# Optimization experiments

Hardware: AMD Instinct MI355X
Metric: run time of the kernel (lower is better)

Reference implementation:

```python
import jax, jax.numpy as jnp
import numpy as np
import math

BS, S, E, H, DK = 32, 512, 512, 8, 64


def setup_inputs() -> dict:
    key = jax.random.key(0)
    ks = jax.random.split(key, 10)
    q = jax.random.normal(ks[0], (BS, S, E), jnp.float32)
    k = jax.random.normal(ks[1], (BS, S, E), jnp.float32)
    v = jax.random.normal(ks[2], (BS, S, E), jnp.float32)
    # strictly-causal mask: allowed where col < row (np.triu(k=0)==0)
    mask = jnp.tril(jnp.ones((S, S), bool), -1)[None, None]
    sc = 1.0 / math.sqrt(E)  # xavier-ish scale for square linears
    Wq = jax.random.normal(ks[3], (E, E), jnp.float32) * sc
    Wk = jax.random.normal(ks[4], (E, E), jnp.float32) * sc
    Wv = jax.random.normal(ks[5], (E, E), jnp.float32) * sc
    Wo = jax.random.normal(ks[6], (E, E), jnp.float32) * sc
    bq = jnp.zeros((E,), jnp.float32)
    bk = jnp.zeros((E,), jnp.float32)
    bv = jnp.zeros((E,), jnp.float32)
    bo = jnp.zeros((E,), jnp.float32)
    gammas = jax.random.normal(ks[7], (H, 1, 1), jnp.float32) * 0.5
    return {"q": q, "k": k, "v": v, "mask": mask, "zero_pad": 1,
            "Wq": Wq, "bq": bq, "Wk": Wk, "bk": bk, "Wv": Wv, "bv": bv,
            "Wo": Wo, "bo": bo, "gammas": gammas}


def reference(q, k, v, mask, zero_pad, Wq, bq, Wk, bk, Wv, bv, Wo, bo, gammas):
    bs = q.shape[0]
    # projections (torch Linear: x @ W.T + b), split heads -> [b,h,s,d]
    def heads(x, W, b):
        return (x @ W.T + b).reshape(bs, S, H, DK).transpose(0, 2, 1, 3)
    qh, kh, vh = heads(q, Wq, bq), heads(k, Wk, bk), heads(v, Wv, bv)

    scores = jnp.einsum('bhqd,bhkd->bhqk', qh, kh) / math.sqrt(DK)

    # --- distance-decay term (no-grad in original) ---
    neg = jnp.float32(-1e32)
    scores_ = jnp.where(mask, scores, neg)
    scores_ = jax.nn.softmax(scores_, axis=-1) * mask.astype(scores.dtype)
    distcum = jnp.cumsum(scores_, axis=-1)
    disttotal = jnp.sum(scores_, axis=-1, keepdims=True)
    idx = jnp.arange(S)
    position_effect = jnp.abs(idx[None, :] - idx[:, None]).astype(scores.dtype)[None, None]
    dist_scores = jnp.sqrt(jnp.clip((disttotal - distcum) * position_effect, 0.0))
    dist_scores = jax.lax.stop_gradient(dist_scores)

    gamma = -jax.nn.softplus(gammas)[None]  # [1,h,1,1]
    total_effect = jnp.clip(jnp.exp(dist_scores * gamma), 1e-5, 1e5)

    scores = scores * total_effect
    scores = jnp.where(mask, scores, neg)
    scores = jax.nn.softmax(scores, axis=-1)
    if zero_pad:
        scores = scores.at[:, :, 0, :].set(0.0)

    out = jnp.einsum('bhqk,bhkd->bhqd', scores, vh)
    concat = out.transpose(0, 2, 1, 3).reshape(bs, S, E)
    return concat @ Wo.T + bo
```

## Files before the change

kernel.cpp:

```cpp
#include <hip/hip_runtime.h>
#include <hip/hip_bf16.h>
#include <hip/hip_fp16.h>
#include <stdint.h>

#define BSZ 32
#define SEQ 512
#define EMB 512
#define NH  8
#define DKD 64
#define LOG2E 1.4426950408889634f

typedef float f32x4 __attribute__((ext_vector_type(4)));
typedef short s16x8 __attribute__((ext_vector_type(8)));

#if __has_builtin(__builtin_amdgcn_exp2f)
#define EXP2(x) __builtin_amdgcn_exp2f(x)
#else
#define EXP2(x) exp2f(x)
#endif
#define RCP(x) __builtin_amdgcn_rcpf(x)

__device__ inline unsigned short f2bf(float f) {
  union { float f; unsigned u; } v; v.f = f;
  unsigned r = v.u + 0x7fffu + ((v.u >> 16) & 1u);
  return (unsigned short)(r >> 16);
}

__device__ inline ushort4 pack4bf(float4 v) {
  union { __hip_bfloat162 h2[2]; ushort4 u4; } cv;
  cv.h2[0] = __float22bfloat162_rn(make_float2(v.x, v.y));
  cv.h2[1] = __float22bfloat162_rn(make_float2(v.z, v.w));
  return cv.u4;
}

__device__ inline void stage16(const void* g, void* l) {
#if defined(__has_builtin) && __has_builtin(__builtin_amdgcn_global_load_lds)
  __builtin_amdgcn_global_load_lds(
      (const __attribute__((address_space(1))) void*)g,
      (__attribute__((address_space(3))) void*)l, 16, 0, 0);
#else
  *reinterpret_cast<uint4*>(l) = *reinterpret_cast<const uint4*>(g);
#endif
}

template<int CTRL>
__device__ inline float dpp_shr_f(float x) {
  return __builtin_bit_cast(float,
    __builtin_amdgcn_update_dpp(0, __builtin_bit_cast(int, x), CTRL, 0xf, 0xf, true));
}
__device__ inline float rlane(float v, int l) {
  return __builtin_bit_cast(float, __builtin_amdgcn_readlane(__builtin_bit_cast(int, v), l));
}

__global__ __launch_bounds__(256)
void wcvt(const float* __restrict__ w0, const float* __restrict__ w1,
          const float* __restrict__ w2, const float* __restrict__ w3,
          unsigned short* __restrict__ o0, unsigned short* __restrict__ o1,
          unsigned short* __restrict__ o2, unsigned short* __restrict__ o3)
{
  const float* src = (blockIdx.y == 0) ? w0 : (blockIdx.y == 1) ? w1
                   : (blockIdx.y == 2) ? w2 : w3;
  unsigned short* dst = (blockIdx.y == 0) ? o0 : (blockIdx.y == 1) ? o1
                      : (blockIdx.y == 2) ? o2 : o3;
  const int i = (blockIdx.x * 256 + threadIdx.x) * 8;
  float4 a = *reinterpret_cast<const float4*>(src + i);
  float4 b = *reinterpret_cast<const float4*>(src + i + 4);
  union { ushort4 p[2]; s16x8 v; } cc;
  cc.p[0] = pack4bf(a); cc.p[1] = pack4bf(b);
  *reinterpret_cast<s16x8*>(dst + i) = cc.v;
}

template<int PROJ>
__global__ __launch_bounds__(256)
void proj_gemm(const float* __restrict__ A, const unsigned short* __restrict__ Bw,
               const float* __restrict__ bias, unsigned short* __restrict__ Out,
               float oscale)
{
  __shared__ __align__(16) char smem[32768];
  char* const sA = smem;
  char* const sB = smem + 16384;
  const int tid  = threadIdx.x;
  const int lane = tid & 63;
  const int w    = tid >> 6;
  const int lin  = blockIdx.x;
  const int x    = lin & 7;
  const int j    = lin >> 3;
  const int pl   = j & 15;
  const int m0   = (x * 16 + pl) * 128;
  const int n0   = (j >> 4) * 128;
  const int K = EMB;

  const int wr   = (w >> 1) * 64;
  const int wc   = (w & 1) * 64;
  const int base = w * 1024 + lane * 16;

  auto stage = [&](int k0) {
    #pragma unroll
    for (int c = 0; c < 4; ++c) {
      const int flat = c * 4096 + base;
      const int row  = flat >> 7;
      const int gl   = ((flat >> 4) & 7) ^ (row & 7);
      stage16(&A[(size_t)(m0 + row) * K + k0 + gl * 4], sA + flat);
    }
    #pragma unroll
    for (int c = 0; c < 2; ++c) {
      const int flat = c * 4096 + base;
      const int r    = flat >> 7;
      const int gl   = ((flat >> 4) & 7) ^ (r & 7);
      const int nn   = r + ((gl >> 2) << 6);
      stage16(&Bw[(size_t)(n0 + nn) * K + k0 + (gl & 3) * 8], sB + flat);
    }
  };

  f32x4 acc[4][4] = {};
  auto compute = [&]() {
    s16x8 af[4], bf[4];
    #pragma unroll
    for (int i = 0; i < 4; ++i) {
      const int row = wr + i * 16 + (lane & 15);
      const int g1  = (lane >> 4) << 1;
      float4 v1 = *reinterpret_cast<const float4*>(sA + row * 128 + ((g1 ^ (row & 7)) << 4));
      float4 v2 = *reinterpret_cast<const float4*>(sA + row * 128 + (((g1 + 1) ^ (row & 7)) << 4));
      union { ushort4 p[2]; s16x8 vv; } cc;
      cc.p[0] = pack4bf(v1); cc.p[1] = pack4bf(v2);
      af[i] = cc.vv;
    }
    #pragma unroll
    for (int jj = 0; jj < 4; ++jj) {
      const int n  = wc + jj * 16 + (lane & 15);
      const int r  = n & 63;
      const int gl = ((n >> 6) << 2) + (lane >> 4);
      bf[jj] = *reinterpret_cast<const s16x8*>(sB + r * 128 + ((gl ^ (r & 7)) << 4));
    }
    #pragma unroll
    for (int i = 0; i < 4; ++i)
      #pragma unroll
      for (int jj = 0; jj < 4; ++jj)
        acc[i][jj] = __builtin_amdgcn_mfma_f32_16x16x32_bf16(af[i], bf[jj], acc[i][jj], 0, 0, 0);
  };

  for (int t = 0; t < 16; ++t) {
    stage(t * 32);
    __syncthreads();
    compute();
    __syncthreads();
  }

  unsigned short* tl = (unsigned short*)smem;
  #pragma unroll
  for (int jj = 0; jj < 4; ++jj) {
    const int n  = wc + jj * 16 + (lane & 15);
    const float bs = bias[n0 + n];
    #pragma unroll
    for (int i = 0; i < 4; ++i)
      #pragma unroll
      for (int r = 0; r < 4; ++r) {
        const int m = wr + i * 16 + (lane >> 4) * 4 + r;
        const unsigned short val = f2bf((acc[i][jj][r] + bs) * oscale);
        const int row = (PROJ == 2) ? n : m;
        const int cb  = (PROJ == 2) ? (m * 2) : (n * 2);
        *(unsigned short*)((char*)tl + row * 256 + (cb ^ ((row & 7) << 4))) = val;
      }
  }
  __syncthreads();
  #pragma unroll
  for (int c = 0; c < 8; ++c) {
    const int flat = c * 4096 + tid * 16;
    const int rowi = flat >> 8;
    const int cb   = flat & 255;
    s16x8 vchunk = *reinterpret_cast<const s16x8*>(
        (char*)tl + rowi * 256 + (cb ^ ((rowi & 7) << 4)));
    size_t dst;
    if (PROJ == 2) {
      const int gn = n0 + rowi;
      const int b  = m0 >> 9, sb = (m0 & 511) + (cb >> 1);
      const int h  = gn >> 6, d = gn & 63;
      dst = ((size_t)(b * NH + h) * DKD + d) * SEQ + sb;
    } else {
      const int gm = m0 + rowi;
      const int gn = n0 + (cb >> 1);
      const int b  = gm >> 9, s = gm & 511;
      const int h  = gn >> 6, d = gn & 63;
      dst = ((size_t)(b * NH + h) * SEQ + s) * DKD + d;
    }
    *reinterpret_cast<s16x8*>(&Out[dst]) = vchunk;
  }
}

__global__ __launch_bounds__(256)
void out_gemm(const unsigned short* __restrict__ At,
              const unsigned short* __restrict__ Wo,
              const float* __restrict__ bo, float* __restrict__ C)
{
  __shared__ __align__(16) char smem[2 * 16384];
  const int tid  = threadIdx.x;
  const int lane = tid & 63;
  const int w    = tid >> 6;
  const int lin  = blockIdx.x;
  const int x    = lin & 7;
  const int j    = lin >> 3;
  const int P    = x * 16 + (j >> 2);
  const int m0   = P * 128;
  const int n0   = (j & 3) * 128;
  const int K = EMB, N = EMB;

  const int wr   = (w >> 1) * 64;
  const int wc   = (w & 1) * 64;
  const int base = w * 1024 + lane * 16;

  auto stage = [&](int buf, int k0) {
    char* sA = smem + buf * 16384;
    char* sB = sA + 8192;
    #pragma unroll
    for (int c = 0; c < 2; ++c) {
      const int flat = c * 4096 + base;
      const int r    = flat >> 7;
      const int gl   = ((flat >> 4) & 7) ^ (r & 7);
      const int row  = r + ((gl >> 2) << 6);
      stage16(&At[(size_t)(m0 + row) * K + k0 + (gl & 3) * 8], sA + flat);
    }
    #pragma unroll
    for (int c = 0; c < 2; ++c) {
      const int flat = c * 4096 + base;
      const int r    = flat >> 7;
      const int gl   = ((flat >> 4) & 7) ^ (r & 7);
      const int nn   = r + ((gl >> 2) << 6);
      stage16(&Wo[(size_t)(n0 + nn) * K + k0 + (gl & 3) * 8], sB + flat);
    }
  };

  f32x4 acc[4][4] = {};
  auto compute = [&](int buf) {
    char* sA = smem + buf * 16384;
    char* sB = sA + 8192;
    s16x8 af[4], bf[4];
    #pragma unroll
    for (int i = 0; i < 4; ++i) {
      const int row = wr + i * 16 + (lane & 15);
      const int r   = row & 63;
      const int gl  = ((row >> 6) << 2) + (lane >> 4);
      af[i] = *reinterpret_cast<const s16x8*>(sA + r * 128 + ((gl ^ (r & 7)) << 4));
    }
    #pragma unroll
    for (int jj = 0; jj < 4; ++jj) {
      const int n  = wc + jj * 16 + (lane & 15);
      const int r  = n & 63;
      const int gl = ((n >> 6) << 2) + (lane >> 4);
      bf[jj] = *reinterpret_cast<const s16x8*>(sB + r * 128 + ((gl ^ (r & 7)) << 4));
    }
    #pragma unroll
    for (int i = 0; i < 4; ++i)
      #pragma unroll
      for (int jj = 0; jj < 4; ++jj)
        acc[i][jj] = __builtin_amdgcn_mfma_f32_16x16x32_bf16(af[i], bf[jj], acc[i][jj], 0, 0, 0);
  };

  stage(0, 0);
  int cur = 0;
  for (int t = 0; t < 15; ++t) {
    stage(cur ^ 1, (t + 1) * 32);
    asm volatile("s_waitcnt vmcnt(4)" ::: "memory");
    __builtin_amdgcn_s_barrier();
    __builtin_amdgcn_sched_barrier(0);
    compute(cur);
    asm volatile("s_waitcnt lgkmcnt(0)" ::: "memory");
    __builtin_amdgcn_s_barrier();
    cur ^= 1;
  }
  asm volatile("s_waitcnt vmcnt(0)" ::: "memory");
  __builtin_amdgcn_s_barrier();
  __builtin_amdgcn_sched_barrier(0);
  compute(cur);

  #pragma unroll
  for (int i = 0; i < 4; ++i)
    #pragma unroll
    for (int jj = 0; jj < 4; ++jj)
      #pragma unroll
      for (int r = 0; r < 4; ++r) {
        const int gm = m0 + wr + i * 16 + (lane >> 4) * 4 + r;
        const int gn = n0 + wc + jj * 16 + (lane & 15);
        C[(size_t)gm * N + gn] = acc[i][jj][r] + bo[gn];
      }
}

template<int R>
__device__ inline void phase2_rows(unsigned short* s_lds, int w, int lane,
                                   int q0, int zp, float g2)
{
  constexpr int L  = 64 / R;
  constexpr int IT = 4 / R;
  const int seg = lane / L;
  const int li  = lane & (L - 1);
  const int jb  = li * 8;
  const float NEGINF = -__builtin_inff();
  #pragma unroll
  for (int it = 0; it < IT; ++it) {
    const int r  = w * 4 + it * R + seg;
    const int qg = q0 + r;
    const int gs = li ^ (r & 7);
    unsigned short* rowp = &s_lds[r * 512 + gs * 8];
    float pn2[8];
    if (qg == 0) {
      const float u = zp ? 0.0f : (1.0f / 512.0f);
      #pragma unroll
      for (int i = 0; i < 8; ++i) pn2[i] = u;
    } else {
      float sL[8];
      {
        s16x8 raw = *reinterpret_cast<const s16x8*>(rowp);
        union { s16x8 v; __half2 h[4]; } u; u.v = raw;
        #pragma unroll
        for (int i = 0; i < 4; ++i) {
          float2 f = __half22float2(u.h[i]);
          sL[2 * i] = f.x; sL[2 * i + 1] = f.y;
        }
      }
      #pragma unroll
      for (int i = 0; i < 8; ++i) sL[i] = (jb + i < qg) ? sL[i] : NEGINF;
      float p[8], c[8];
      float run = 0.f;
      #pragma unroll
      for (int i = 0; i < 8; ++i) { p[i] = EXP2(sL[i]); run += p[i]; c[i] = run; }
      float t = run;
      t += dpp_shr_f<0x111>(t);
      t += dpp_shr_f<0x112>(t);
      t += dpp_shr_f<0x114>(t);
      t += dpp_shr_f<0x118>(t);
      float tot;
      if constexpr (R == 1) {
        const float r0 = rlane(t, 15), r1 = rlane(t, 31), r2 = rlane(t, 47);
        const float a1 = r0, a2 = r0 + r1, a3 = a2 + r2;
        tot = a3 + rlane(t, 63);
        t += (lane >= 48) ? a3 : (lane >= 32) ? a2 : (lane >= 16) ? a1 : 0.f;
      } else if constexpr (R == 2) {
        const float r0 = rlane(t, 15), r2 = rlane(t, 47);
        t += (lane & 16) ? ((lane < 32) ? r0 : r2) : 0.f;
        tot = __shfl(t, lane | 31, 64);
      } else {
        tot = __shfl(t, lane | 15, 64);
      }
      const float pre  = tot - (t - run);
      const float g2r  = g2 * __builtin_amdgcn_sqrtf(RCP(tot));
      const float fb   = (float)(qg - jb);
      float p2[8]; float run2 = 0.f;
      #pragma unroll
      for (int i = 0; i < 8; ++i) {
        const float rem = pre - c[i];
        const float arg = fmaxf(rem * (fb - (float)i), 0.f);
        float te = EXP2(__builtin_amdgcn_sqrtf(arg) * g2r);
        te = fmaxf(te, 1e-5f);
        p2[i] = EXP2(sL[i] * te);
        run2 += p2[i];
      }
      float y = run2;
      y += dpp_shr_f<0x111>(y);
      y += dpp_shr_f<0x112>(y);
      y += dpp_shr_f<0x114>(y);
      y += dpp_shr_f<0x118>(y);
      float s2;
      if constexpr (R == 1) {
        s2 = rlane(y, 15) + rlane(y, 31) + rlane(y, 47) + rlane(y, 63);
      } else if constexpr (R == 2) {
        y += (lane & 16) ? ((lane < 32) ? rlane(y, 15) : rlane(y, 47)) : 0.f;
        s2 = __shfl(y, lane | 31, 64);
      } else {
        s2 = __shfl(y, lane | 15, 64);
      }
      const float inv2 = RCP(s2);
      #pragma unroll
      for (int i = 0; i < 8; ++i) pn2[i] = p2[i] * inv2;
    }
    union { __hip_bfloat162 h2[4]; uint4 u; } pk;
    pk.h2[0] = __float22bfloat162_rn(make_float2(pn2[0], pn2[1]));
    pk.h2[1] = __float22bfloat162_rn(make_float2(pn2[2], pn2[3]));
    pk.h2[2] = __float22bfloat162_rn(make_float2(pn2[4], pn2[5]));
    pk.h2[3] = __float22bfloat162_rn(make_float2(pn2[6], pn2[7]));
    *reinterpret_cast<uint4*>(rowp) = pk.u;
  }
}

__global__ __launch_bounds__(256)
void attn_kernel(const unsigned short* __restrict__ Qh,
                 const unsigned short* __restrict__ Kh,
                 const unsigned short* __restrict__ Vt,
                 unsigned short* __restrict__ Aout,
                 const float* __restrict__ gammas,
                 const int* __restrict__ zero_pad)
{
  __shared__ __align__(16) unsigned short s_lds[16 * 512];
  const int tid = threadIdx.x, lane = tid & 63, w = tid >> 6;
  const int lin = blockIdx.x;
  const int x   = lin & 7;
  const int u   = lin >> 3;
  const int qb  = u >> 5;
  const int h   = u & 7;
  const int b   = x * 4 + ((u >> 3) & 3);
  const int q0  = qb * 16;
  const size_t bh = (size_t)b * NH + h;
  const unsigned short* Qp = Qh + bh * SEQ * DKD;
  const unsigned short* Kp = Kh + bh * SEQ * DKD;
  const unsigned short* Vp = Vt + bh * DKD * SEQ;
  const int zp = zero_pad[0];
  const float g2 = -log1pf(__expf(gammas[h])) * LOG2E;

  s16x8 aq[2];
  #pragma unroll
  for (int kt = 0; kt < 2; ++kt)
    aq[kt] = *reinterpret_cast<const s16x8*>(&Qp[(q0 + (lane & 15)) * DKD + kt * 32 + (lane >> 4) * 8]);
  {
    const int frag = (lane >> 4) * 8;
    auto loadK = [&](int t, s16x8* kb) {
      const int n = t * 16 + (lane & 15);
      kb[0] = *reinterpret_cast<const s16x8*>(&Kp[n * DKD + frag]);
      kb[1] = *reinterpret_cast<const s16x8*>(&Kp[n * DKD + 32 + frag]);
    };
    auto tilecomp = [&](int t, const s16x8* kb) {
      f32x4 acc = {};
      acc = __builtin_amdgcn_mfma_f32_16x16x32_bf16(aq[0], kb[0], acc, 0, 0, 0);
      acc = __builtin_amdgcn_mfma_f32_16x16x32_bf16(aq[1], kb[1], acc, 0, 0, 0);
      const int n = t * 16 + (lane & 15);
      #pragma unroll
      for (int r = 0; r < 4; ++r) {
        const int row = (lane >> 4) * 4 + r;
        const int idx = row * 512 + ((((n >> 3) ^ (row & 7)) << 3) + (n & 7));
        s_lds[idx] = __half_as_ushort(__float2half(acc[r]));
      }
    };
    int t = w;
    if (t <= qb) {
      s16x8 cur[2], nxt[2];
      loadK(t, cur);
      while (true) {
        const int tn = t + 4;
        if (tn <= qb) {
          loadK(tn, nxt);
          tilecomp(t, cur);
          cur[0] = nxt[0]; cur[1] = nxt[1];
          t = tn;
        } else {
          tilecomp(t, cur);
          break;
        }
      }
    }
  }
  __syncthreads();

  if (zp == 0 && qb == 0) {
    phase2_rows<1>(s_lds, w, lane, q0, zp, g2);
  } else if (qb < 8) {
    phase2_rows<4>(s_lds, w, lane, q0, zp, g2);
  } else if (qb < 16) {
    phase2_rows<2>(s_lds, w, lane, q0, zp, g2);
  } else {
    phase2_rows<1>(s_lds, w, lane, q0, zp, g2);
  }
  __syncthreads();

  f32x4 oacc = {};
  const int row  = lane & 15;
  const int koff = lane >> 4;
  const int rsw  = row & 7;
  const unsigned short* vbase = &Vp[(w * 16 + row) * SEQ + koff * 8];
  const int ks_end = (qb == 0 && zp == 0) ? 16 : (qb >> 1) + 1;
  int ks0 = 0;
  for (; ks0 + 4 <= ks_end; ks0 += 4) {
    s16x8 vb[4], pa[4];
    #pragma unroll
    for (int uu = 0; uu < 4; ++uu) {
      const int ks = ks0 + uu;
      vb[uu] = *reinterpret_cast<const s16x8*>(&vbase[ks * 32]);
      pa[uu] = *reinterpret_cast<const s16x8*>(&s_lds[row * 512 + ((ks * 4 + koff) ^ rsw) * 8]);
    }
    #pragma unroll
    for (int uu = 0; uu < 4; ++uu)
      oacc = __builtin_amdgcn_mfma_f32_16x16x32_bf16(pa[uu], vb[uu], oacc, 0, 0, 0);
  }
  for (; ks0 < ks_end; ++ks0) {
    s16x8 vb = *reinterpret_cast<const s16x8*>(&vbase[ks0 * 32]);
    s16x8 pa = *reinterpret_cast<const s16x8*>(&s_lds[row * 512 + ((ks0 * 4 + koff) ^ rsw) * 8]);
    oacc = __builtin_amdgcn_mfma_f32_16x16x32_bf16(pa, vb, oacc, 0, 0, 0);
  }
  #pragma unroll
  for (int r = 0; r < 4; ++r) {
    const int orow = (lane >> 4) * 4 + r;
    const int ocol = w * 16 + (lane & 15);
    Aout[((size_t)b * SEQ + (q0 + orow)) * EMB + h * DKD + ocol] = f2bf(oacc[r]);
  }
}

extern "C" void kernel_launch(void* const* d_in, const int* in_sizes, int n_in,
                              void* d_out, int out_size, void* d_ws, size_t ws_size,
                              hipStream_t stream)
{
  const float* q  = (const float*)d_in[0];
  const float* k  = (const float*)d_in[1];
  const float* v  = (const float*)d_in[2];
  const int*   zp = (const int*)d_in[4];
  const float* Wq = (const float*)d_in[5];
  const float* bq = (const float*)d_in[6];
  const float* Wk = (const float*)d_in[7];
  const float* bk = (const float*)d_in[8];
  const float* Wv = (const float*)d_in[9];
  const float* bv = (const float*)d_in[10];
  const float* Wo = (const float*)d_in[11];
  const float* bo = (const float*)d_in[12];
  const float* gm = (const float*)d_in[13];

  char* ws = (char*)d_ws;
  const size_t HB = (size_t)BSZ * NH * SEQ * DKD * sizeof(unsigned short);
  const size_t WB = (size_t)EMB * EMB * sizeof(unsigned short);
  unsigned short* Qh  = (unsigned short*)(ws);
  unsigned short* Kh  = (unsigned short*)(ws + HB);
  unsigned short* Vt  = (unsigned short*)(ws + 2 * HB);
  unsigned short* At  = (unsigned short*)(ws + 3 * HB);
  unsigned short* Wqb = (unsigned short*)(ws + 4 * HB);
  unsigned short* Wkb = (unsigned short*)(ws + 4 * HB + WB);
  unsigned short* Wvb = (unsigned short*)(ws + 4 * HB + 2 * WB);
  unsigned short* Wob = (unsigned short*)(ws + 4 * HB + 3 * WB);

  wcvt<<<dim3(128, 4), 256, 0, stream>>>(Wq, Wk, Wv, Wo, Wqb, Wkb, Wvb, Wob);
  proj_gemm<0><<<512, 256, 0, stream>>>(q, Wqb, bq, Qh, 0.125f * LOG2E);
  proj_gemm<1><<<512, 256, 0, stream>>>(k, Wkb, bk, Kh, 1.0f);
  proj_gemm<2><<<512, 256, 0, stream>>>(v, Wvb, bv, Vt, 1.0f);
  attn_kernel<<<8192, 256, 0, stream>>>(Qh, Kh, Vt, At, gm, zp);
  out_gemm<<<512, 256, 0, stream>>>(At, Wob, bo, (float*)d_out);
}
```

Before: 155.3 us.

## Double-buffer projection GEMM staging and halve M tile to double grid

The projection GEMM now uses two shared-memory buffers so the next K-slice is loaded while the current one is computed, with explicit vmcnt waits and barriers in place of two full syncthreads per step. The M tile shrinks from 128 to 64 rows, which doubles the block count to 1024 for better occupancy and CU coverage. The aim is to hide global-load latency in the three projection kernels. The cost is less reuse of each B tile per block and more manual synchronisation that depends on the exact count of outstanding loads.

```diff
diff --git a/kernel.cpp b/kernel.cpp
--- a/kernel.cpp
+++ b/kernel.cpp
@@ -76,27 +76,28 @@
                const float* __restrict__ bias, unsigned short* __restrict__ Out,
                float oscale)
 {
-  __shared__ __align__(16) char smem[32768];
-  char* const sA = smem;
-  char* const sB = smem + 16384;
+  __shared__ __align__(16) char smem[2 * 16384];
   const int tid  = threadIdx.x;
   const int lane = tid & 63;
   const int w    = tid >> 6;
   const int lin  = blockIdx.x;
   const int x    = lin & 7;
-  const int j    = lin >> 3;
-  const int pl   = j & 15;
-  const int m0   = (x * 16 + pl) * 128;
-  const int n0   = (j >> 4) * 128;
+  const int u    = lin >> 3;
+  const int panel= x * 32 + (u & 31);
+  const int nb   = u >> 5;
+  const int m0   = panel * 64;
+  const int n0   = nb * 128;
   const int K = EMB;
 
-  const int wr   = (w >> 1) * 64;
+  const int wr   = (w >> 1) * 32;
   const int wc   = (w & 1) * 64;
   const int base = w * 1024 + lane * 16;
 
-  auto stage = [&](int k0) {
-    #pragma unroll
-    for (int c = 0; c < 4; ++c) {
+  auto stage = [&](int buf, int k0) {
+    char* sA = smem + buf * 16384;
+    char* sB = sA + 8192;
+    #pragma unroll
+    for (int c = 0; c < 2; ++c) {
       const int flat = c * 4096 + base;
       const int row  = flat >> 7;
       const int gl   = ((flat >> 4) & 7) ^ (row & 7);
@@ -112,11 +113,13 @@
     }
   };
 
-  f32x4 acc[4][4] = {};
-  auto compute = [&]() {
-    s16x8 af[4], bf[4];
-    #pragma unroll
-    for (int i = 0; i < 4; ++i) {
+  f32x4 acc[2][4] = {};
+  auto compute = [&](int buf) {
+    char* sA = smem + buf * 16384;
+    char* sB = sA + 8192;
+    s16x8 af[2], bf[4];
+    #pragma unroll
+    for (int i = 0; i < 2; ++i) {
       const int row = wr + i * 16 + (lane & 15);
       const int g1  = (lane >> 4) << 1;
       float4 v1 = *reinterpret_cast<const float4*>(sA + row * 128 + ((g1 ^ (row & 7)) << 4));
@@ -133,50 +136,65 @@
       bf[jj] = *reinterpret_cast<const s16x8*>(sB + r * 128 + ((gl ^ (r & 7)) << 4));
     }
     #pragma unroll
-    for (int i = 0; i < 4; ++i)
+    for (int i = 0; i < 2; ++i)
       #pragma unroll
       for (int jj = 0; jj < 4; ++jj)
         acc[i][jj] = __builtin_amdgcn_mfma_f32_16x16x32_bf16(af[i], bf[jj], acc[i][jj], 0, 0, 0);
   };
 
-  for (int t = 0; t < 16; ++t) {
-    stage(t * 32);
-    __syncthreads();
-    compute();
-    __syncthreads();
-  }
-
-  unsigned short* tl = (unsigned short*)smem;
+  stage(0, 0);
+  int cur = 0;
+  for (int t = 0; t < 15; ++t) {
+    stage(cur ^ 1, (t + 1) * 32);
+    asm volatile("s_waitcnt vmcnt(4)" ::: "memory");
+    __builtin_amdgcn_s_barrier();
+    __builtin_amdgcn_sched_barrier(0);
+    compute(cur);
+    asm volatile("s_waitcnt lgkmcnt(0)" ::: "memory");
+    __builtin_amdgcn_s_barrier();
+    cur ^= 1;
+  }
+  asm volatile("s_waitcnt vmcnt(0)" ::: "memory");
+  __builtin_amdgcn_s_barrier();
+  __builtin_amdgcn_sched_barrier(0);
+  compute(cur);
+  __syncthreads();
+
+  char* const tl = smem;
   #pragma unroll
   for (int jj = 0; jj < 4; ++jj) {
     const int n  = wc + jj * 16 + (lane & 15);
     const float bs = bias[n0 + n];
     #pragma unroll
-    for (int i = 0; i < 4; ++i)
+    for (int i = 0; i < 2; ++i)
       #pragma unroll
       for (int r = 0; r < 4; ++r) {
         const int m = wr + i * 16 + (lane >> 4) * 4 + r;
         const unsigned short val = f2bf((acc[i][jj][r] + bs) * oscale);
-        const int row = (PROJ == 2) ? n : m;
-        const int cb  = (PROJ == 2) ? (m * 2) : (n * 2);
-        *(unsigned short*)((char*)tl + row * 256 + (cb ^ ((row & 7) << 4))) = val;
+        if (PROJ == 2)
+          *(unsigned short*)(tl + n * 128 + ((m * 2) ^ ((n & 7) << 4))) = val;
+        else
+          *(unsigned short*)(tl + m * 256 + ((n * 2) ^ ((m & 7) << 4))) = val;
       }
   }
   __syncthreads();
   #pragma unroll
-  for (int c = 0; c < 8; ++c) {
+  for (int c = 0; c < 4; ++c) {
     const int flat = c * 4096 + tid * 16;
-    const int rowi = flat >> 8;
-    const int cb   = flat & 255;
-    s16x8 vchunk = *reinterpret_cast<const s16x8*>(
-        (char*)tl + rowi * 256 + (cb ^ ((rowi & 7) << 4)));
     size_t dst;
+    s16x8 vchunk;
     if (PROJ == 2) {
+      const int rowi = flat >> 7;
+      const int cb   = flat & 127;
+      vchunk = *reinterpret_cast<const s16x8*>(tl + rowi * 128 + (cb ^ ((rowi & 7) << 4)));
       const int gn = n0 + rowi;
       const int b  = m0 >> 9, sb = (m0 & 511) + (cb >> 1);
       const int h  = gn >> 6, d = gn & 63;
       dst = ((size_t)(b * NH + h) * DKD + d) * SEQ + sb;
     } else {
+      const int rowi = flat >> 8;
+      const int cb   = flat & 255;
+      vchunk = *reinterpret_cast<const s16x8*>(tl + rowi * 256 + (cb ^ ((rowi & 7) << 4)));
       const int gm = m0 + rowi;
       const int gn = n0 + (cb >> 1);
       const int b  = gm >> 9, s = gm & 511;
@@ -521,9 +539,9 @@
   unsigned short* Wob = (unsigned short*)(ws + 4 * HB + 3 * WB);
 
   wcvt<<<dim3(128, 4), 256, 0, stream>>>(Wq, Wk, Wv, Wo, Wqb, Wkb, Wvb, Wob);
-  proj_gemm<0><<<512, 256, 0, stream>>>(q, Wqb, bq, Qh, 0.125f * LOG2E);
-  proj_gemm<1><<<512, 256, 0, stream>>>(k, Wkb, bk, Kh, 1.0f);
-  proj_gemm<2><<<512, 256, 0, stream>>>(v, Wvb, bv, Vt, 1.0f);
+  proj_gemm<0><<<1024, 256, 0, stream>>>(q, Wqb, bq, Qh, 0.125f * LOG2E);
+  proj_gemm<1><<<1024, 256, 0, stream>>>(k, Wkb, bk, Kh, 1.0f);
+  proj_gemm<2><<<1024, 256, 0, stream>>>(v, Wvb, bv, Vt, 1.0f);
   attn_kernel<<<8192, 256, 0, stream>>>(Qh, Kh, Vt, At, gm, zp);
   out_gemm<<<512, 256, 0, stream>>>(At, Wob, bo, (float*)d_out);
 }
```

Result: no change. 155.5 us (+0.1%).
